# Kernel optimization log

Measured on AMD Instinct MI355X. Metric: run time of the kernel, lower is better.

## Reference

```python
import jax, jax.numpy as jnp
import numpy as np

EPS = 1e-05           # COFT radius
R_BLOCKS = 16         # number of orthogonal blocks
DEQ_SCALE = 0.01      # dequant scale multiplier (keeps activations O(1))


def _project_batch(R, eps):
    # peft OFT project_batch: projects each block onto Frobenius ball of
    # radius eps/sqrt(n_blocks) around the ZERO matrix (peft uses zeros, not eye)
    eps = eps / jnp.sqrt(jnp.asarray(R.shape[0], R.dtype))
    norm = jnp.sqrt(jnp.sum(R * R, axis=(1, 2), keepdims=True))
    proj = eps * R / norm
    return jnp.where(norm <= eps, R, proj)


def _cayley_batch(R):
    # Q = (I - skew) @ inv(I + skew), skew = 0.5*(R - R^T), batched over blocks
    b = R.shape[-1]
    skew = 0.5 * (R - jnp.swapaxes(R, -1, -2))
    I = jnp.eye(b, dtype=R.dtype)
    return jnp.matmul(I - skew, jnp.linalg.inv(I + skew))


def setup_inputs() -> dict:
    key = jax.random.key(0)
    k1, k2, k3, k4, k5 = jax.random.split(key, 5)
    B, S, IN, OUT = 4, 1024, 4096, 4096
    blk = IN // R_BLOCKS
    x = jax.random.normal(k1, (B, S, IN), dtype=jnp.float32)
    qweight = jax.random.randint(k2, (OUT, IN), 0, 256, dtype=jnp.int32)
    scales = jax.random.uniform(k3, (OUT,), dtype=jnp.float32)
    bias = jax.random.normal(k4, (OUT,), dtype=jnp.float32)
    oft_R = jax.random.normal(k5, (R_BLOCKS, blk, blk), dtype=jnp.float32)
    return {"x": x, "qweight": qweight, "scales": scales, "bias": bias, "oft_R": oft_R}


def reference(x, qweight, scales, bias, oft_R):
    # 1) dequantize base weight (per-out-channel scale, zero point 128)
    W = (qweight.astype(jnp.float32) - 128.0) * (scales[:, None] * DEQ_SCALE)  # [out, in]

    # 2) COFT projection (done under no_grad in torch -> straight-through here)
    Rp = oft_R + jax.lax.stop_gradient(_project_batch(oft_R, EPS) - oft_R)

    # 3) Cayley transform per block -> orthogonal blocks [r, b, b]
    Q = _cayley_batch(Rp)
    r, b, _ = Q.shape
    out_f, in_f = W.shape

    # 4) block-diagonal @ W^T, done block-wise (never materialize [in,in])
    Wt = W.T.reshape(r, b, out_f)                       # fix_filt blocks [r, b, out]
    filt = jnp.einsum('rij,rjo->rio', Q, Wt).reshape(in_f, out_f).T  # [out, in]

    # 5) linear with rotated weight (torch forward overwrites the base result)
    return jnp.einsum('bsi,oi->bso', x, filt) + bias
```

## Files before the change

### kernel.cpp

```cpp
#include <hip/hip_runtime.h>

typedef __attribute__((ext_vector_type(4))) int i32x4;
typedef __attribute__((ext_vector_type(16))) int i32x16;

#define XSCALE (5.0f / 127.0f)
#define XINV   (127.0f / 5.0f)


__global__ void quant_x_t(const float* __restrict__ x, char* __restrict__ x8,
                          long nsl, int K, int NKT) {
    long stride = (long)gridDim.x * blockDim.x;
    for (long s = (long)blockIdx.x * blockDim.x + threadIdx.x; s < nsl; s += stride) {
        long c = s >> 6; int l = (int)(s & 63);
        int rb = (int)(c / NKT);
        int U  = (int)(c - (long)rb * NKT);
        int row = (rb << 5) + (l & 31);
        int k0  = (U << 5) + ((l >> 5) << 4);
        const float* src = x + (size_t)row * K + k0;
        unsigned w[4];
#pragma unroll
        for (int q = 0; q < 4; ++q) {
            float4 v = *(const float4*)(src + q * 4);
            unsigned b0 = (unsigned char)(signed char)(int)rintf(fminf(fmaxf(v.x * XINV, -127.f), 127.f));
            unsigned b1 = (unsigned char)(signed char)(int)rintf(fminf(fmaxf(v.y * XINV, -127.f), 127.f));
            unsigned b2 = (unsigned char)(signed char)(int)rintf(fminf(fmaxf(v.z * XINV, -127.f), 127.f));
            unsigned b3 = (unsigned char)(signed char)(int)rintf(fminf(fmaxf(v.w * XINV, -127.f), 127.f));
            w[q] = b0 | (b1 << 8) | (b2 << 16) | (b3 << 24);
        }
        i32x4 o; o[0] = (int)w[0]; o[1] = (int)w[1]; o[2] = (int)w[2]; o[3] = (int)w[3];
        *(i32x4*)(x8 + s * 16) = o;
    }
}

__global__ void prep_w8(const int* __restrict__ q, char* __restrict__ w8,
                        long nsl, int K, int NKT) {
    long stride = (long)gridDim.x * blockDim.x;
    for (long s = (long)blockIdx.x * blockDim.x + threadIdx.x; s < nsl; s += stride) {
        long c = s >> 6; int l = (int)(s & 63);
        int rb = (int)(c / NKT);
        int U  = (int)(c - (long)rb * NKT);
        int row = (rb << 5) + (l & 31);
        int k0  = (U << 5) + ((l >> 5) << 4);
        const int* src = q + (size_t)row * K + k0;
        unsigned w[4];
#pragma unroll
        for (int t = 0; t < 4; ++t) {
            int4 v = *(const int4*)(src + t * 4);
            unsigned b0 = (unsigned char)(signed char)(v.x - 128);
            unsigned b1 = (unsigned char)(signed char)(v.y - 128);
            unsigned b2 = (unsigned char)(signed char)(v.z - 128);
            unsigned b3 = (unsigned char)(signed char)(v.w - 128);
            w[t] = b0 | (b1 << 8) | (b2 << 16) | (b3 << 24);
        }
        i32x4 o; o[0] = (int)w[0]; o[1] = (int)w[1]; o[2] = (int)w[2]; o[3] = (int)w[3];
        *(i32x4*)(w8 + s * 16) = o;
    }
}

#define GLDS(d_, o_, b_) asm volatile("global_load_dwordx4 %0, %1, %2" \
                                      : "=v"(d_) : "v"(o_), "s"(b_))
#define VMCNT(n_)  asm volatile("s_waitcnt vmcnt(" #n_ ")" ::: "memory")
#define SB0        __builtin_amdgcn_sched_barrier(0)

__global__ __launch_bounds__(256, 2) void gemm_nb(
    const char* __restrict__ A, const char* __restrict__ Bt,
    const float* __restrict__ so, const float* __restrict__ bias,
    float* __restrict__ C, int M, int N, int K) {
    const int NKT = K >> 5;
    int tid = threadIdx.x;
    int nbn = N >> 7;
    int nwg = gridDim.x;
    int bid = blockIdx.x;
    if ((nwg & 7) == 0) {
        int cpx = nwg >> 3;
        bid = (bid & 7) * cpx + (bid >> 3);
    }
    int bm = (bid / nbn) << 8;
    int bn = (bid % nbn) << 7;

    int wv = tid >> 6, l = tid & 63;
    int rl = l & 31, g2 = l >> 5;
    int wm = wv >> 1, wn = wv & 1;

    int rb0 = (bm >> 5) + 4 * wm;
    int nb0 = (bn >> 5) + 2 * wn;
    unsigned lo = (unsigned)(l * 16);
    unsigned oA0 = (unsigned)(rb0 + 0) * (unsigned)(NKT * 1024) + lo;
    unsigned oA1 = (unsigned)(rb0 + 1) * (unsigned)(NKT * 1024) + lo;
    unsigned oA2 = (unsigned)(rb0 + 2) * (unsigned)(NKT * 1024) + lo;
    unsigned oA3 = (unsigned)(rb0 + 3) * (unsigned)(NKT * 1024) + lo;
    unsigned oB0 = (unsigned)(nb0 + 0) * (unsigned)(NKT * 1024) + lo;
    unsigned oB1 = (unsigned)(nb0 + 1) * (unsigned)(NKT * 1024) + lo;

    i32x16 acc[4][2] = {};
    i32x4 aX[4], bX[2], aY[4], bY[2], aZ[4], bZ[2];

#define LOADN(AB_, BB_) {                                                            \
    GLDS(AB_[0], oA0, A); GLDS(AB_[1], oA1, A);                                      \
    GLDS(AB_[2], oA2, A); GLDS(AB_[3], oA3, A);                                      \
    GLDS(BB_[0], oB0, Bt); GLDS(BB_[1], oB1, Bt);                                    \
    oA0 += 1024; oA1 += 1024; oA2 += 1024; oA3 += 1024;                              \
    oB0 += 1024; oB1 += 1024; }

#define MFMA8(AB_, BB_)                                                              \
    __builtin_amdgcn_s_setprio(1);                                                   \
    _Pragma("unroll") for (int m_ = 0; m_ < 4; ++m_) {                               \
        acc[m_][0] = __builtin_amdgcn_mfma_i32_32x32x32_i8(                          \
            AB_[m_], BB_[0], acc[m_][0], 0, 0, 0);                                   \
        acc[m_][1] = __builtin_amdgcn_mfma_i32_32x32x32_i8(                          \
            AB_[m_], BB_[1], acc[m_][1], 0, 0, 0); }                                 \
    __builtin_amdgcn_s_setprio(0);

    LOADN(aX, bX)
    LOADN(aY, bY)
    LOADN(aZ, bZ)

    int T = 0;
    for (; T + 5 < NKT; T += 3) {
        VMCNT(12); SB0; MFMA8(aX, bX) LOADN(aX, bX)
        VMCNT(12); SB0; MFMA8(aY, bY) LOADN(aY, bY)
        VMCNT(12); SB0; MFMA8(aZ, bZ) LOADN(aZ, bZ)
    }
    VMCNT(12); SB0; MFMA8(aX, bX) LOADN(aX, bX)
    VMCNT(12); SB0; MFMA8(aY, bY) LOADN(aY, bY)
    VMCNT(12); SB0; MFMA8(aZ, bZ)
    VMCNT(6);  SB0; MFMA8(aX, bX)
    VMCNT(0);  SB0; MFMA8(aY, bY)

    int col0 = bn + wn * 64 + rl;
    int row0 = bm + wm * 128 + 4 * g2;
#pragma unroll
    for (int n = 0; n < 2; ++n) {
        int col = col0 + n * 32;
        float bv = bias[col];
        float sc = so[col] * 0.01f * XSCALE;
#pragma unroll
        for (int m = 0; m < 4; ++m) {
            int rowm = row0 + m * 32;
#pragma unroll
            for (int r = 0; r < 16; ++r) {
                int row = rowm + (r & 3) + 8 * (r >> 2);
                C[(size_t)row * N + col] = (float)acc[m][n][r] * sc + bv;
            }
        }
    }
#undef LOADN
#undef MFMA8
}

__global__ __launch_bounds__(256) void gemm_fallback(
    const float* __restrict__ x, const int* __restrict__ q,
    const float* __restrict__ scales, const float* __restrict__ bias,
    float* __restrict__ C, int M, int N, int K) {
    __shared__ float As[64][16];
    __shared__ float Bs[64][17];
    int tid = threadIdx.x;
    int nbn = N >> 6;
    int bm = (blockIdx.x / nbn) << 6;
    int bn = (blockIdx.x % nbn) << 6;
    int tx = tid & 15, ty = tid >> 4;
    int lr = tid >> 2, lc = (tid & 3) << 2;
    float acc[4][4] = {};
    for (int k0 = 0; k0 < K; k0 += 16) {
        float4 av = *(const float4*)(x + (size_t)(bm + lr) * K + k0 + lc);
        As[lr][lc] = av.x; As[lr][lc + 1] = av.y; As[lr][lc + 2] = av.z; As[lr][lc + 3] = av.w;
        int4 qv = *(const int4*)(q + (size_t)(bn + lr) * K + k0 + lc);
        float s = scales[bn + lr] * 0.01f;
        Bs[lr][lc] = (qv.x - 128) * s; Bs[lr][lc + 1] = (qv.y - 128) * s;
        Bs[lr][lc + 2] = (qv.z - 128) * s; Bs[lr][lc + 3] = (qv.w - 128) * s;
        __syncthreads();
#pragma unroll
        for (int kk = 0; kk < 16; kk++) {
            float a[4], b[4];
#pragma unroll
            for (int i = 0; i < 4; i++) a[i] = As[ty * 4 + i][kk];
#pragma unroll
            for (int j = 0; j < 4; j++) b[j] = Bs[tx * 4 + j][kk];
#pragma unroll
            for (int i = 0; i < 4; i++)
#pragma unroll
                for (int j = 0; j < 4; j++) acc[i][j] += a[i] * b[j];
        }
        __syncthreads();
    }
#pragma unroll
    for (int i = 0; i < 4; i++)
#pragma unroll
        for (int j = 0; j < 4; j++) {
            int row = bm + ty * 4 + i, col = bn + tx * 4 + j;
            C[(size_t)row * N + col] = acc[i][j] + bias[col];
        }
}

extern "C" void kernel_launch(void* const* d_in, const int* in_sizes, int n_in,
                              void* d_out, int out_size, void* d_ws, size_t ws_size,
                              hipStream_t stream) {
    const float* x      = (const float*)d_in[0];
    const int*   qw     = (const int*)d_in[1];
    const float* scales = (const float*)d_in[2];
    const float* bias   = (const float*)d_in[3];
    float* out = (float*)d_out;

    int OUT = in_sizes[2];
    int IN  = in_sizes[1] / OUT;
    int M   = in_sizes[0] / IN;
    int NKT = IN >> 5;

    size_t szX8 = (size_t)M * IN;
    size_t szW8 = (size_t)OUT * IN;
    size_t need = szX8 + szW8;
    if (ws_size >= need && (M % 256) == 0 && (OUT % 128) == 0 &&
        (IN % 32) == 0 && NKT >= 5 && (NKT % 3) == 2) {
        char* x8 = (char*)d_ws;
        char* w8 = x8 + szX8;
        quant_x_t<<<2048, 256, 0, stream>>>(x, x8, (long)M * IN / 16, IN, NKT);
        prep_w8<<<2048, 256, 0, stream>>>(qw, w8, (long)OUT * IN / 16, IN, NKT);
        dim3 grid((M / 256) * (OUT / 128));
        gemm_nb<<<grid, 256, 0, stream>>>(x8, w8, scales, bias, out, M, OUT, IN);
    } else {
        dim3 grid((M / 64) * (OUT / 64));
        gemm_fallback<<<grid, 256, 0, stream>>>(x, qw, scales, bias, out, M, OUT, IN);
    }
}
```

Before: 103.9 us.

## Stage A tiles through LDS with async global_load_lds triple buffering

The int8 GEMM now streams each wave's A fragments from global memory straight into a per-wave triple-buffered LDS region using global_load_lds, then reads them back with ds_read_b128. B fragments are still loaded into registers, with double buffering. The goal is to cut VGPR pressure from holding three sets of A registers and to keep deeper prefetch in flight. The cost is extra LDS traffic and lgkmcnt waits before each MFMA group, and the dispatch condition now requires an even K-tile count.

Result: slower. 115.4 us (+11.1%).

```diff
diff --git a/kernel.cpp b/kernel.cpp
--- a/kernel.cpp
+++ b/kernel.cpp
@@ -57,15 +57,29 @@
     }
 }
 
+__device__ __forceinline__ void gld_lds16(const char* g, char* l) {
+    __builtin_amdgcn_global_load_lds(
+        (const __attribute__((address_space(1))) void*)g,
+        (__attribute__((address_space(3))) void*)l, 16, 0, 0);
+}
+
+__device__ __forceinline__ unsigned lds_addr(const char* p) {
+    return (unsigned)(unsigned long long)(const __attribute__((address_space(3))) char*)p;
+}
+
+#define DSR(d_, b_, o_) asm volatile("ds_read_b128 %0, %1 offset:" #o_ : "=v"(d_) : "v"(b_))
 #define GLDS(d_, o_, b_) asm volatile("global_load_dwordx4 %0, %1, %2" \
                                       : "=v"(d_) : "v"(o_), "s"(b_))
 #define VMCNT(n_)  asm volatile("s_waitcnt vmcnt(" #n_ ")" ::: "memory")
+#define LGKM0      asm volatile("s_waitcnt lgkmcnt(0)" ::: "memory")
 #define SB0        __builtin_amdgcn_sched_barrier(0)
 
-__global__ __launch_bounds__(256, 2) void gemm_nb(
+__global__ __launch_bounds__(256, 2) void gemm_pw(
     const char* __restrict__ A, const char* __restrict__ Bt,
     const float* __restrict__ so, const float* __restrict__ bias,
     float* __restrict__ C, int M, int N, int K) {
+    __shared__ __align__(16) char As[4 * 12288];
+
     const int NKT = K >> 5;
     int tid = threadIdx.x;
     int nbn = N >> 7;
@@ -83,49 +97,66 @@
     int wm = wv >> 1, wn = wv & 1;
 
     int rb0 = (bm >> 5) + 4 * wm;
+    const char* pA0 = A + (size_t)(rb0 + 0) * NKT * 1024 + l * 16;
+    const char* pA1 = A + (size_t)(rb0 + 1) * NKT * 1024 + l * 16;
+    const char* pA2 = A + (size_t)(rb0 + 2) * NKT * 1024 + l * 16;
+    const char* pA3 = A + (size_t)(rb0 + 3) * NKT * 1024 + l * 16;
     int nb0 = (bn >> 5) + 2 * wn;
     unsigned lo = (unsigned)(l * 16);
-    unsigned oA0 = (unsigned)(rb0 + 0) * (unsigned)(NKT * 1024) + lo;
-    unsigned oA1 = (unsigned)(rb0 + 1) * (unsigned)(NKT * 1024) + lo;
-    unsigned oA2 = (unsigned)(rb0 + 2) * (unsigned)(NKT * 1024) + lo;
-    unsigned oA3 = (unsigned)(rb0 + 3) * (unsigned)(NKT * 1024) + lo;
     unsigned oB0 = (unsigned)(nb0 + 0) * (unsigned)(NKT * 1024) + lo;
     unsigned oB1 = (unsigned)(nb0 + 1) * (unsigned)(NKT * 1024) + lo;
 
+    char* ldsW = As + wv * 12288;
+    unsigned aBase = lds_addr(As) + wv * 12288 + l * 16;
+
     i32x16 acc[4][2] = {};
-    i32x4 aX[4], bX[2], aY[4], bY[2], aZ[4], bZ[2];
-
-#define LOADN(AB_, BB_) {                                                            \
-    GLDS(AB_[0], oA0, A); GLDS(AB_[1], oA1, A);                                      \
-    GLDS(AB_[2], oA2, A); GLDS(AB_[3], oA3, A);                                      \
-    GLDS(BB_[0], oB0, Bt); GLDS(BB_[1], oB1, Bt);                                    \
-    oA0 += 1024; oA1 += 1024; oA2 += 1024; oA3 += 1024;                              \
-    oB0 += 1024; oB1 += 1024; }
-
-#define MFMA8(AB_, BB_)                                                              \
-    __builtin_amdgcn_s_setprio(1);                                                   \
-    _Pragma("unroll") for (int m_ = 0; m_ < 4; ++m_) {                               \
-        acc[m_][0] = __builtin_amdgcn_mfma_i32_32x32x32_i8(                          \
-            AB_[m_], BB_[0], acc[m_][0], 0, 0, 0);                                   \
-        acc[m_][1] = __builtin_amdgcn_mfma_i32_32x32x32_i8(                          \
-            AB_[m_], BB_[1], acc[m_][1], 0, 0, 0); }                                 \
+    i32x4 aE[4], aO[4], bE[2], bO[2];
+
+#define STAGE(STEL_) {                                                             \
+    char* d = ldsW + (STEL_);                                                      \
+    gld_lds16(pA0, d);        gld_lds16(pA1, d + 1024);                            \
+    gld_lds16(pA2, d + 2048); gld_lds16(pA3, d + 3072);                            \
+    pA0 += 1024; pA1 += 1024; pA2 += 1024; pA3 += 1024; }
+
+#define BLOAD(BB_) { GLDS(BB_[0], oB0, Bt); GLDS(BB_[1], oB1, Bt);                 \
+                     oB0 += 1024; oB1 += 1024; }
+
+#define MFMA8(AB_, BB_)                                                            \
+    __builtin_amdgcn_s_setprio(1);                                                 \
+    _Pragma("unroll") for (int m_ = 0; m_ < 4; ++m_) {                             \
+        acc[m_][0] = __builtin_amdgcn_mfma_i32_32x32x32_i8(                        \
+            AB_[m_], BB_[0], acc[m_][0], 0, 0, 0);                                 \
+        acc[m_][1] = __builtin_amdgcn_mfma_i32_32x32x32_i8(                        \
+            AB_[m_], BB_[1], acc[m_][1], 0, 0, 0); }                               \
     __builtin_amdgcn_s_setprio(0);
 
-    LOADN(aX, bX)
-    LOADN(aY, bY)
-    LOADN(aZ, bZ)
+#define ITER(AF_, BC_, BN_, DOB_, DOS_, VM_) {                                     \
+    VM_; SB0;                                                                      \
+    unsigned ab = aBase + sB;                                                      \
+    DSR(AF_[0], ab, 0);    DSR(AF_[1], ab, 1024);                                  \
+    DSR(AF_[2], ab, 2048); DSR(AF_[3], ab, 3072);                                  \
+    if (DOB_) { BLOAD(BN_) }                                                       \
+    if (DOS_) { STAGE(stEl) }                                                      \
+    LGKM0; SB0;                                                                    \
+    MFMA8(AF_, BC_)                                                                \
+    sB   = (sB   == 8192u) ? 0u : sB + 4096u;                                      \
+    stEl = (stEl == 8192u) ? 0u : stEl + 4096u;                                    \
+}
+
+    STAGE(0)
+    BLOAD(bE)
+    STAGE(4096)
+
+    unsigned sB = 0;
+    unsigned stEl = 8192;
 
     int T = 0;
-    for (; T + 5 < NKT; T += 3) {
-        VMCNT(12); SB0; MFMA8(aX, bX) LOADN(aX, bX)
-        VMCNT(12); SB0; MFMA8(aY, bY) LOADN(aY, bY)
-        VMCNT(12); SB0; MFMA8(aZ, bZ) LOADN(aZ, bZ)
-    }
-    VMCNT(12); SB0; MFMA8(aX, bX) LOADN(aX, bX)
-    VMCNT(12); SB0; MFMA8(aY, bY) LOADN(aY, bY)
-    VMCNT(12); SB0; MFMA8(aZ, bZ)
-    VMCNT(6);  SB0; MFMA8(aX, bX)
-    VMCNT(0);  SB0; MFMA8(aY, bY)
+    for (; T + 3 < NKT; T += 2) {
+        ITER(aE, bE, bO, 1, 1, VMCNT(4))
+        ITER(aO, bO, bE, 1, 1, VMCNT(4))
+    }
+    ITER(aE, bE, bO, 1, 0, VMCNT(4))
+    ITER(aO, bO, bE, 0, 0, VMCNT(0))
 
     int col0 = bn + wn * 64 + rl;
     int row0 = bm + wm * 128 + 4 * g2;
@@ -144,8 +175,10 @@
             }
         }
     }
-#undef LOADN
+#undef STAGE
+#undef BLOAD
 #undef MFMA8
+#undef ITER
 }
 
 __global__ __launch_bounds__(256) void gemm_fallback(
@@ -210,13 +243,13 @@
     size_t szW8 = (size_t)OUT * IN;
     size_t need = szX8 + szW8;
     if (ws_size >= need && (M % 256) == 0 && (OUT % 128) == 0 &&
-        (IN % 32) == 0 && NKT >= 5 && (NKT % 3) == 2) {
+        (IN % 32) == 0 && NKT >= 6 && (NKT % 2) == 0) {
         char* x8 = (char*)d_ws;
         char* w8 = x8 + szX8;
         quant_x_t<<<2048, 256, 0, stream>>>(x, x8, (long)M * IN / 16, IN, NKT);
         prep_w8<<<2048, 256, 0, stream>>>(qw, w8, (long)OUT * IN / 16, IN, NKT);
         dim3 grid((M / 256) * (OUT / 128));
-        gemm_nb<<<grid, 256, 0, stream>>>(x8, w8, scales, bias, out, M, OUT, IN);
+        gemm_pw<<<grid, 256, 0, stream>>>(x8, w8, scales, bias, out, M, OUT, IN);
     } else {
         dim3 grid((M / 64) * (OUT / 64));
         gemm_fallback<<<grid, 256, 0, stream>>>(x, qw, scales, bias, out, M, OUT, IN);
```
